# Kernel tuning notes

Hardware: AMD Instinct MI355X
Metric: run time of the kernel (lower is better)

## Reference

```python
import jax, jax.numpy as jnp
import numpy as np
from jax import lax

B = 8; DIM = 256; NH = 8; PATCH = 8; WS = 28; STRIDE = 8; PAD = 14; ORF = 2.0; IMG = 448


def conv2d(x, w, stride, pad, groups=1):
    return lax.conv_general_dilated(
        x, w, (stride, stride), [(pad, pad), (pad, pad)],
        dimension_numbers=('NCHW', 'OIHW', 'NCHW'), feature_group_count=groups)


def ln_ch(x, g, b):
    # LayerNormProxy: LayerNorm over channel dim of NCHW
    m = jnp.mean(x, 1, keepdims=True)
    v = jnp.mean((x - m) ** 2, 1, keepdims=True)
    return (x - m) * lax.rsqrt(v + 1e-5) * g[None, :, None, None] + b[None, :, None, None]


def bilinear_sample(x, grid):
    # x: (N,C,H,W); grid: (N,Hg,Wg,2) in (x,y) order, [-1,1], align_corners=True, zeros padding
    N, C, H, W = x.shape
    gx = (grid[..., 0] + 1.0) * 0.5 * (W - 1)
    gy = (grid[..., 1] + 1.0) * 0.5 * (H - 1)
    x0 = jnp.floor(gx); y0 = jnp.floor(gy)
    x1 = x0 + 1.0; y1 = y0 + 1.0
    wx1 = gx - x0; wx0 = 1.0 - wx1
    wy1 = gy - y0; wy0 = 1.0 - wy1
    xf = x.reshape(N, C, H * W)

    def corner(ix, iy, w):
        valid = (ix >= 0) & (ix <= W - 1) & (iy >= 0) & (iy <= H - 1)
        ii = (jnp.clip(iy, 0, H - 1) * W + jnp.clip(ix, 0, W - 1)).astype(jnp.int32).reshape(N, -1)
        vals = jax.vmap(lambda f, i: f[:, i])(xf, ii)  # (N,C,Hg*Wg)
        return vals * (w * valid).reshape(N, 1, -1)

    out = (corner(x0, y0, wx0 * wy0) + corner(x1, y0, wx1 * wy0)
           + corner(x0, y1, wx0 * wy1) + corner(x1, y1, wx1 * wy1))
    return out.reshape(N, C, grid.shape[1], grid.shape[2])


def setup_inputs() -> dict:
    key = jax.random.key(0)
    ks = jax.random.split(key, 12)
    s = 0.02
    CG = 64
    return {
        'x': jax.random.normal(ks[0], (B, 3, IMG, IMG), jnp.float32),
        'patch_w': jax.random.normal(ks[1], (DIM, 3, PATCH, PATCH), jnp.float32) * s,
        'patch_b': jnp.zeros((DIM,), jnp.float32),
        'ln1_g': jnp.ones((DIM,), jnp.float32),
        'ln1_b': jnp.zeros((DIM,), jnp.float32),
        'wq': jax.random.normal(ks[2], (DIM, DIM), jnp.float32) * s,
        'bq': jnp.zeros((DIM,), jnp.float32),
        'wk': jax.random.normal(ks[3], (DIM, DIM), jnp.float32) * s,
        'bk': jnp.zeros((DIM,), jnp.float32),
        'wv': jax.random.normal(ks[4], (DIM, DIM), jnp.float32) * s,
        'bv': jnp.zeros((DIM,), jnp.float32),
        'wo': jax.random.normal(ks[5], (DIM, DIM), jnp.float32) * s,
        'bo': jnp.zeros((DIM,), jnp.float32),
        'off_dw_w': jax.random.normal(ks[6], (CG, 1, WS, WS), jnp.float32) * s,
        'off_dw_b': jnp.zeros((CG,), jnp.float32),
        'off_ln_g': jnp.ones((CG,), jnp.float32),
        'off_ln_b': jnp.zeros((CG,), jnp.float32),
        'off_pw_w': jax.random.normal(ks[7], (2, CG), jnp.float32) * s,
        'rpe_w1': jax.random.normal(ks[8], (32, 2), jnp.float32) * 0.1,
        'rpe_b1': jnp.zeros((32,), jnp.float32),
        'rpe_w2': jax.random.normal(ks[9], (2, 32), jnp.float32) * 0.1,
    }


def reference(x, patch_w, patch_b, ln1_g, ln1_b, wq, bq, wk, bk, wv, bv, wo, bo,
              off_dw_w, off_dw_b, off_ln_g, off_ln_b, off_pw_w, rpe_w1, rpe_b1, rpe_w2):
    Bn = x.shape[0]
    # patch embedding: Conv2d(3, dim, patch, patch) + LayerNormProxy
    feat = conv2d(x, patch_w, PATCH, 0) + patch_b[None, :, None, None]
    feat = ln_ch(feat, ln1_g, ln1_b)
    H, W = feat.shape[2], feat.shape[3]  # 56, 56
    G = (H // WS) * (W // WS)            # 4 groups
    CG = DIM // G; GH = NH // G; HC = DIM // NH
    # q projection (1x1 conv)
    q = jnp.einsum('oc,bchw->bohw', wq, feat) + bq[None, :, None, None]
    # offset network on per-group query features
    q_off = q.reshape(Bn * G, CG, H, W)
    off = conv2d(q_off, off_dw_w, STRIDE, PAD, groups=CG) + off_dw_b[None, :, None, None]
    off = jax.nn.gelu(ln_ch(off, off_ln_g, off_ln_b), approximate=False)
    off = jnp.einsum('oc,bchw->bohw', off_pw_w, off)   # (B*G, 2, Hk, Wk)
    Hk, Wk = off.shape[2], off.shape[3]
    ns = Hk * Wk
    rng = jnp.array([1.0 / (Hk - 1), 1.0 / (Wk - 1)], off.dtype).reshape(1, 2, 1, 1)
    offset = jnp.tanh(off) * rng * ORF
    offset = jnp.transpose(offset, (0, 2, 3, 1))  # (B*G, Hk, Wk, 2) in (y, x)
    # reference points, normalized to ~[-1, 1]
    ry = jnp.linspace(0.5, Hk - 0.5, Hk) / (Hk - 1) * 2.0 - 1.0
    rx = jnp.linspace(0.5, Wk - 0.5, Wk) / (Wk - 1) * 2.0 - 1.0
    ref = jnp.stack(jnp.meshgrid(ry, rx, indexing='ij'), -1)  # (Hk, Wk, 2)
    ref = jnp.broadcast_to(ref[None], (Bn * G, Hk, Wk, 2))
    pos = offset + ref
    # deformable sampling (grid expects (x, y) order)
    xs = bilinear_sample(feat.reshape(Bn * G, CG, H, W), pos[..., ::-1])  # (B*G, CG, Hk, Wk)
    xs = xs.reshape(Bn, DIM, ns)
    k = jnp.einsum('oc,bcn->bon', wk, xs) + bk[None, :, None]
    v = jnp.einsum('oc,bcn->bon', wv, xs) + bv[None, :, None]
    qh = q.reshape(Bn * NH, HC, H * W)
    kh = k.reshape(Bn * NH, HC, ns)
    vh = v.reshape(Bn * NH, HC, ns)
    attn = jnp.einsum('bcm,bcn->bmn', qh, kh) * (HC ** -0.5)  # (B*NH, HW, ns)
    # log-CPB relative position bias
    qy = jnp.linspace(0.0, float(H), H) / (H - 1) * 2.0 - 1.0
    qx = jnp.linspace(0.0, float(W), W) / (W - 1) * 2.0 - 1.0
    qg = jnp.stack(jnp.meshgrid(qy, qx, indexing='ij'), -1).reshape(H * W, 2)
    disp = (qg[None, :, None, :] - pos.reshape(Bn * G, ns, 2)[:, None, :, :]) * 4.0
    disp = jnp.sign(disp) * jnp.log2(jnp.abs(disp) + 1.0) / 3.0  # /log2(8)
    bias = jax.nn.relu(jnp.einsum('bmnc,hc->bmnh', disp, rpe_w1) + rpe_b1)
    bias = jnp.einsum('bmnh,oh->bmno', bias, rpe_w2)  # (B*G, HW, ns, GH)
    attn = attn + jnp.transpose(bias, (0, 3, 1, 2)).reshape(Bn * NH, H * W, ns)
    attn = jax.nn.softmax(attn, axis=-1)
    out = jnp.einsum('bmn,bcn->bcm', attn, vh).reshape(Bn, DIM, H, W)
    y = jnp.einsum('oc,bchw->bohw', wo, out) + bo[None, :, None, None]
    return (y, pos.reshape(Bn, G, Hk, Wk, 2), ref.reshape(Bn, G, Hk, Wk, 2))
```

## Files before the change

### kernel.cpp

```cpp
#include <hip/hip_runtime.h>
#include <cstddef>


typedef short bf16x8 __attribute__((ext_vector_type(8)));
typedef float f32x4 __attribute__((ext_vector_type(4)));

static __device__ __forceinline__ ushort f2bf(float f) {
  union { float f; unsigned u; } v; v.f = f;
  unsigned r = v.u + 0x7fffu + ((v.u >> 16) & 1u);
  return (ushort)(r >> 16);
}
static __device__ __forceinline__ float bf2f(ushort u) {
  union { unsigned u; float f; } v; v.u = ((unsigned)u) << 16;
  return v.f;
}

#define OFF_FEATB 0u
#define OFF_QPK   3211264u
#define OFF_Q     6422528u
#define OFF_POS   12845056u
#define OFF_XS    12849152u
#define OFF_KPK   12980224u
#define OFF_VPK   13045760u
#define OFF_PWP   13111296u
#define OFF_WQP   13135872u
#define OFF_WOP   13168640u
#define OFF_WKT   13201408u
#define OFF_WVT   13266944u

__global__ __launch_bounds__(256) void k_xcvt(
    const float* __restrict__ x, ushort* __restrict__ xb) {
  const size_t i0 = ((size_t)blockIdx.x * 256 + threadIdx.x) * 8;
  float4 v0 = *(const float4*)(x + i0);
  float4 v1 = *(const float4*)(x + i0 + 4);
  bf16x8 o;
  o[0] = (short)f2bf(v0.x); o[1] = (short)f2bf(v0.y);
  o[2] = (short)f2bf(v0.z); o[3] = (short)f2bf(v0.w);
  o[4] = (short)f2bf(v1.x); o[5] = (short)f2bf(v1.y);
  o[6] = (short)f2bf(v1.z); o[7] = (short)f2bf(v1.w);
  *(bf16x8*)(xb + i0) = o;
}

__global__ __launch_bounds__(256) void k_pack(
    const float* __restrict__ pw, const float* __restrict__ wq,
    const float* __restrict__ wk, const float* __restrict__ wv,
    const float* __restrict__ wo, ushort* __restrict__ pwp,
    ushort* __restrict__ wqp, ushort* __restrict__ wop,
    float* __restrict__ wkT, float* __restrict__ wvT) {
  const int o = blockIdx.x, t = threadIdx.x, m = blockIdx.y;
  if (m == 0) {
    if (t < 192) pwp[((t >> 3) * 256 + o) * 8 + (t & 7)] = f2bf(pw[o * 192 + t]);
  } else if (m == 1) {
    wqp[((t >> 3) * 256 + o) * 8 + (t & 7)] = f2bf(wq[o * 256 + t]);
  } else if (m == 2) {
    wop[((t >> 3) * 256 + o) * 8 + (t & 7)] = f2bf(wo[o * 256 + t]);
  } else if (m == 3) {
    wkT[t * 256 + o] = wk[o * 256 + t];
  } else {
    wvT[t * 256 + o] = wv[o * 256 + t];
  }
}

__global__ __launch_bounds__(256) void k_patch_mfma(
    const ushort* __restrict__ xb, const ushort* __restrict__ pwp,
    const float* __restrict__ pb, const float* __restrict__ g1,
    const float* __restrict__ b1, ushort* __restrict__ featb) {
  const int t = threadIdx.x;
  const int lane = t & 63;
  const int wid = t >> 6;
  const int m_base = blockIdx.x * 64 + wid * 16;
  const int kg = lane >> 4;
  const int lr = lane & 15;
  const int mA = m_base + lr;
  const int bA = mA / 3136;
  const int posA = mA - bA * 3136;
  const int ohA = posA / 56;
  const int owA = posA - ohA * 56;

  f32x4 acc[16];
#pragma unroll
  for (int f = 0; f < 16; f++) {
    float bv = pb[f * 16 + lr];
    acc[f] = (f32x4){bv, bv, bv, bv};
  }
#pragma unroll
  for (int ks = 0; ks < 6; ks++) {
    const int k8 = ks * 4 + kg;
    const int ci = k8 >> 3, ii = k8 & 7;
    bf16x8 a = *(const bf16x8*)(xb +
        (((size_t)bA * 3 + ci) * 448 + (ohA * 8 + ii)) * 448 + owA * 8);
#pragma unroll
    for (int f = 0; f < 16; f++) {
      bf16x8 bfr = *(const bf16x8*)(pwp + (size_t)(k8 * 256 + f * 16 + lr) * 8);
      acc[f] = __builtin_amdgcn_mfma_f32_16x16x32_bf16(a, bfr, acc[f], 0, 0, 0);
    }
  }
  float mean[4], rstd[4];
#pragma unroll
  for (int j = 0; j < 4; j++) {
    float s1 = 0.f, s2 = 0.f;
#pragma unroll
    for (int f = 0; f < 16; f++) { float v = acc[f][j]; s1 += v; s2 += v * v; }
#pragma unroll
    for (int off = 8; off >= 1; off >>= 1) {
      s1 += __shfl_xor(s1, off);
      s2 += __shfl_xor(s2, off);
    }
    float mn = s1 * (1.f / 256.f);
    float var = s2 * (1.f / 256.f) - mn * mn;
    mean[j] = mn; rstd[j] = rsqrtf(var + 1e-5f);
  }
#pragma unroll
  for (int f = 0; f < 16; f++) {
    const int c = f * 16 + lr;
    const float gg = g1[c], bb = b1[c];
#pragma unroll
    for (int j = 0; j < 4; j++) {
      const int mo = m_base + kg * 4 + j;
      float v = (acc[f][j] - mean[j]) * rstd[j] * gg + bb;
      featb[(size_t)mo * 256 + c] = f2bf(v);
    }
  }
}

__global__ __launch_bounds__(512) void k_gemm_mfma(
    const ushort* __restrict__ apk, const ushort* __restrict__ wp,
    const float* __restrict__ bias, float* __restrict__ out,
    ushort* __restrict__ opk) {
  const int t = threadIdx.x;
  const int lane = t & 63;
  const int wid = t >> 6;
  const int mt = wid >> 1, nh = wid & 1;
  const int lr = lane & 15, kg = lane >> 4;
  const int m_base = blockIdx.x * 64 + mt * 16;
  const int mA = m_base + lr;

  f32x4 acc[8];
#pragma unroll
  for (int f = 0; f < 8; f++) {
    float bv = bias[nh * 128 + f * 16 + lr];
    acc[f] = (f32x4){bv, bv, bv, bv};
  }
  const ushort* arow = apk + (size_t)mA * 256;
#pragma unroll
  for (int ks = 0; ks < 8; ks++) {
    bf16x8 a = *(const bf16x8*)(arow + ks * 32 + kg * 8);
#pragma unroll
    for (int f = 0; f < 8; f++) {
      const int o = nh * 128 + f * 16 + lr;
      bf16x8 bfr = *(const bf16x8*)(wp + (size_t)((ks * 4 + kg) * 256 + o) * 8);
      acc[f] = __builtin_amdgcn_mfma_f32_16x16x32_bf16(a, bfr, acc[f], 0, 0, 0);
    }
  }
  __shared__ float sA[64 * 257];
#pragma unroll
  for (int f = 0; f < 8; f++) {
#pragma unroll
    for (int j = 0; j < 4; j++)
      sA[(mt * 16 + kg * 4 + j) * 257 + nh * 128 + f * 16 + lr] = acc[f][j];
  }
  __syncthreads();
  const int b = (blockIdx.x * 64) / 3136;
  const int pos0 = (blockIdx.x * 64) % 3136;
#pragma unroll
  for (int i = 0; i < 32; i++) {
    int idx = t + i * 512;
    int c = idx >> 6, mm = idx & 63;
    out[((size_t)b * 256 + c) * 3136 + pos0 + mm] = sA[mm * 257 + c];
  }
  if (opk) {
    const int mm = t & 63;
    const int cs = t >> 6;
#pragma unroll
    for (int i = 0; i < 4; i++) {
      int c0 = cs * 32 + i * 8;
      bf16x8 v8;
#pragma unroll
      for (int j = 0; j < 8; j++) v8[j] = (short)f2bf(sA[mm * 257 + c0 + j]);
      *(bf16x8*)(opk + ((size_t)(blockIdx.x * 64 + mm)) * 256 + c0) = v8;
    }
  }
}

__global__ __launch_bounds__(128) void k_offset_conv(
    const float* __restrict__ q, const float* __restrict__ dww,
    float* __restrict__ convo) {
  const int bg = blockIdx.y;
  const int wv = threadIdx.x >> 6;
  const int lane = threadIdx.x & 63;
  const int ch = blockIdx.x * 2 + wv;
  const int b = bg >> 2, g = bg & 3;

  __shared__ float pl[2][7072];
  float* P = pl[wv];
  for (int idx = lane; idx < 7072; idx += 64) P[idx] = 0.f;

  const float* qb = q + ((size_t)b * 256 + g * 64 + ch) * 3136;
  if (lane < 56) {
    for (int r = 0; r < 56; r++) {
      int hr = r + 14;
      P[hr * 84 + (lane + 14) + (hr >> 3)] = qb[r * 56 + lane];
    }
  }
  const int oh = lane >> 3, ow = lane & 7;
  const int chs = __builtin_amdgcn_readfirstlane(ch);
  const float* wr = dww + (size_t)chs * 784;
  float acc = 0.f;
  const int r0 = oh * 8, c0 = ow * 8;
  for (int i = 0; i < 28; i++) {
    int hr = r0 + i;
    const float* prow = P + hr * 84 + c0 + (hr >> 3);
    const float* wrr = wr + i * 28;
#pragma unroll
    for (int j = 0; j < 28; j++)
      acc = fmaf(prow[j], wrr[j], acc);
  }
  convo[bg * 4096 + lane * 64 + ch] = acc;
}

__global__ __launch_bounds__(256) void k_offset_post(
    const float* __restrict__ convo, const float* __restrict__ dwb,
    const float* __restrict__ lng, const float* __restrict__ lnb,
    const float* __restrict__ pww, float* __restrict__ pos_ws,
    float* __restrict__ out_pos, float* __restrict__ out_ref) {
  const int bg = blockIdx.y;
  const int wv = threadIdx.x >> 6;
  const int lane = threadIdx.x & 63;
  const int idx = blockIdx.x * 4 + wv;
  const int oh = idx >> 3, ow = idx & 7;

  float acc = convo[bg * 4096 + idx * 64 + lane] + dwb[lane];

  float s1 = acc, s2 = acc * acc;
#pragma unroll
  for (int off = 32; off >= 1; off >>= 1) {
    s1 += __shfl_xor(s1, off);
    s2 += __shfl_xor(s2, off);
  }
  float m = s1 * (1.f / 64.f);
  float var = s2 * (1.f / 64.f) - m * m;
  float val = (acc - m) * rsqrtf(var + 1e-5f) * lng[lane] + lnb[lane];
  val = 0.5f * val * (1.f + erff(val * 0.70710678118654752f));
  float p0 = pww[lane] * val, p1 = pww[64 + lane] * val;
#pragma unroll
  for (int off = 32; off >= 1; off >>= 1) {
    p0 += __shfl_xor(p0, off);
    p1 += __shfl_xor(p1, off);
  }
  if (lane == 0) {
    float offy = tanhf(p0) * (2.0f / 7.0f);
    float offx = tanhf(p1) * (2.0f / 7.0f);
    float ry = (0.5f + oh) * (2.0f / 7.0f) - 1.0f;
    float rx = (0.5f + ow) * (2.0f / 7.0f) - 1.0f;
    float py = offy + ry, px = offx + rx;
    int o = bg * 128 + idx * 2;
    pos_ws[o] = py;  pos_ws[o + 1] = px;
    out_pos[o] = py; out_pos[o + 1] = px;
    out_ref[o] = ry; out_ref[o + 1] = rx;
  }
}

__global__ __launch_bounds__(256) void k_sample_kv(
    const ushort* __restrict__ featb, const float* __restrict__ pos_ws,
    const float* __restrict__ wkT, const float* __restrict__ bk,
    const float* __restrict__ wvT, const float* __restrict__ bv,
    ushort* __restrict__ kpk, ushort* __restrict__ vpk) {
  const int b = blockIdx.y;
  const int n = blockIdx.x;
  const int t = threadIdx.x;
  const int g = t >> 6, lane = t & 63;
  const int bg = b * 4 + g;

  __shared__ float sxs[256];
  {
    float py = pos_ws[bg * 128 + n * 2];
    float px = pos_ws[bg * 128 + n * 2 + 1];
    float gx = (px + 1.f) * 0.5f * 55.f;
    float gy = (py + 1.f) * 0.5f * 55.f;
    float x0f = floorf(gx), y0f = floorf(gy);
    int x0 = (int)x0f, y0 = (int)y0f;
    float wx1 = gx - x0f, wx0 = 1.f - wx1;
    float wy1 = gy - y0f, wy0 = 1.f - wy1;
    const size_t mb = (size_t)b * 3136;
    const int cofs = g * 64 + lane;
    float acc = 0.f;
    if (x0 >= 0 && x0 <= 55 && y0 >= 0 && y0 <= 55)
      acc = fmaf(bf2f(featb[(mb + y0 * 56 + x0) * 256 + cofs]), wx0 * wy0, acc);
    if (x0 + 1 >= 0 && x0 + 1 <= 55 && y0 >= 0 && y0 <= 55)
      acc = fmaf(bf2f(featb[(mb + y0 * 56 + x0 + 1) * 256 + cofs]), wx1 * wy0, acc);
    if (x0 >= 0 && x0 <= 55 && y0 + 1 >= 0 && y0 + 1 <= 55)
      acc = fmaf(bf2f(featb[(mb + (y0 + 1) * 56 + x0) * 256 + cofs]), wx0 * wy1, acc);
    if (x0 + 1 >= 0 && x0 + 1 <= 55 && y0 + 1 >= 0 && y0 + 1 <= 55)
      acc = fmaf(bf2f(featb[(mb + (y0 + 1) * 56 + x0 + 1) * 256 + cofs]), wx1 * wy1, acc);
    sxs[g * 64 + lane] = acc;
  }
  __syncthreads();

  float ak = bk[t], av = bv[t];
  for (int c = 0; c < 256; c++) {
    float xv = sxs[c];
    ak = fmaf(wkT[c * 256 + t], xv, ak);
    av = fmaf(wvT[c * 256 + t], xv, av);
  }
  const int h = t >> 5, cc = t & 31;
  const size_t base = (size_t)(b * 8 + h) * 2048;
  kpk[base + (size_t)((cc >> 3) * 64 + n) * 8 + (cc & 7)] = f2bf(ak);
  vpk[base + (size_t)((n >> 3) * 32 + cc) * 8 + (n & 7)] = f2bf(av);
}

__global__ __launch_bounds__(256) void k_attn_mfma(
    const ushort* __restrict__ qpk, const ushort* __restrict__ kpk,
    const ushort* __restrict__ vpk, const float* __restrict__ pos_ws,
    const float* __restrict__ w1, const float* __restrict__ b1,
    const float* __restrict__ w2, ushort* __restrict__ attnpk) {
  const int bg = blockIdx.y;
  const int b = bg >> 2, g = bg & 3;
  const int m0 = blockIdx.x * 64;
  const int t = threadIdx.x;
  const int lane = t & 63, w = t >> 6;
  const int lr = lane & 15, kg = lane >> 4;

  __shared__ ushort Pbuf[4][16 * 72];
  __shared__ ushort outb[64 * 72];
  __shared__ float posl[128];
  __shared__ float4 rpe4[32];
  __shared__ float rpeB[32];

  if (t < 128) posl[t] = pos_ws[bg * 128 + t];
  if (t < 32) {
    rpe4[t] = make_float4(w1[t * 2], w1[t * 2 + 1], b1[t], w2[t]);
    rpeB[t] = w2[32 + t];
  }
  __syncthreads();

  float qgy[4], qgx[4];
#pragma unroll
  for (int j = 0; j < 4; j++) {
    int m = m0 + w * 16 + kg * 4 + j;
    int my = m / 56, mx = m % 56;
    qgy[j] = (float)my * (56.0f / 55.0f) * (2.0f / 55.0f) - 1.0f;
    qgx[j] = (float)mx * (56.0f / 55.0f) * (2.0f / 55.0f) - 1.0f;
  }
  float tyv[16], txv[16];
#pragma unroll
  for (int nf = 0; nf < 4; nf++) {
    int n = nf * 16 + lr;
    float py = posl[2 * n], px = posl[2 * n + 1];
#pragma unroll
    for (int j = 0; j < 4; j++) {
      float dy = (qgy[j] - py) * 4.f;
      float dx = (qgx[j] - px) * 4.f;
      tyv[nf * 4 + j] = copysignf(__log2f(fabsf(dy) + 1.f) * (1.f / 3.f), dy);
      txv[nf * 4 + j] = copysignf(__log2f(fabsf(dx) + 1.f) * (1.f / 3.f), dx);
    }
  }
  float bb0[16], bb1[16];
#pragma unroll
  for (int p = 0; p < 16; p++) { bb0[p] = 0.f; bb1[p] = 0.f; }
  for (int jj = 0; jj < 32; jj++) {
    float4 r = rpe4[jj];
    float wb = rpeB[jj];
#pragma unroll
    for (int p = 0; p < 16; p++) {
      float hv = fmaxf(fmaf(r.x, tyv[p], fmaf(r.y, txv[p], r.z)), 0.f);
      bb0[p] = fmaf(r.w, hv, bb0[p]);
      bb1[p] = fmaf(wb, hv, bb1[p]);
    }
  }

  const int mrow = m0 + w * 16 + lr;
  const float scale = 0.17677669529663687f;
  ushort* pb = Pbuf[w];

  f32x4 oacc[2][2];
#pragma unroll
  for (int gh = 0; gh < 2; gh++)
#pragma unroll
    for (int cf = 0; cf < 2; cf++) oacc[gh][cf] = (f32x4){0.f, 0.f, 0.f, 0.f};

#pragma unroll
  for (int gh = 0; gh < 2; gh++) {
    bf16x8 a = *(const bf16x8*)(qpk +
        ((size_t)(b * 3136 + mrow) * 256 + g * 64 + gh * 32 + kg * 8));
    const ushort* kbase = kpk + (size_t)(b * 8 + g * 2 + gh) * 2048;
    f32x4 s[4];
#pragma unroll
    for (int nf = 0; nf < 4; nf++) {
      bf16x8 bfr = *(const bf16x8*)(kbase + (size_t)(kg * 64 + nf * 16 + lr) * 8);
      s[nf] = __builtin_amdgcn_mfma_f32_16x16x32_bf16(
          a, bfr, (f32x4){0.f, 0.f, 0.f, 0.f}, 0, 0, 0);
    }
#pragma unroll
    for (int nf = 0; nf < 4; nf++)
#pragma unroll
      for (int j = 0; j < 4; j++)
        s[nf][j] = fmaf(s[nf][j], scale,
                        gh ? bb1[nf * 4 + j] : bb0[nf * 4 + j]);
#pragma unroll
    for (int j = 0; j < 4; j++) {
      float m1 = fmaxf(fmaxf(s[0][j], s[1][j]), fmaxf(s[2][j], s[3][j]));
#pragma unroll
      for (int o = 8; o >= 1; o >>= 1) m1 = fmaxf(m1, __shfl_xor(m1, o));
      float ss = 0.f;
#pragma unroll
      for (int nf = 0; nf < 4; nf++) {
        float e = __expf(s[nf][j] - m1);
        s[nf][j] = e;
        ss += e;
      }
#pragma unroll
      for (int o = 8; o >= 1; o >>= 1) ss += __shfl_xor(ss, o);
      float inv = 1.f / ss;
#pragma unroll
      for (int nf = 0; nf < 4; nf++) s[nf][j] *= inv;
    }
#pragma unroll
    for (int nf = 0; nf < 4; nf++)
#pragma unroll
      for (int j = 0; j < 4; j++)
        pb[(kg * 4 + j) * 72 + nf * 16 + lr] = f2bf(s[nf][j]);
    const ushort* vbase = vpk + (size_t)(b * 8 + g * 2 + gh) * 2048;
#pragma unroll
    for (int ks = 0; ks < 2; ks++) {
      bf16x8 pa = *(const bf16x8*)(pb + lr * 72 + ks * 32 + kg * 8);
#pragma unroll
      for (int cf = 0; cf < 2; cf++) {
        bf16x8 vb = *(const bf16x8*)(vbase +
            (size_t)((ks * 4 + kg) * 32 + cf * 16 + lr) * 8);
        oacc[gh][cf] = __builtin_amdgcn_mfma_f32_16x16x32_bf16(
            pa, vb, oacc[gh][cf], 0, 0, 0);
      }
    }
  }

#pragma unroll
  for (int gh = 0; gh < 2; gh++)
#pragma unroll
    for (int cf = 0; cf < 2; cf++)
#pragma unroll
      for (int j = 0; j < 4; j++)
        outb[(w * 16 + kg * 4 + j) * 72 + gh * 32 + cf * 16 + lr] =
            f2bf(oacc[gh][cf][j]);
  __syncthreads();
#pragma unroll
  for (int r2 = 0; r2 < 2; r2++) {
    int row = (t >> 3) + r2 * 32;
    int chunk = t & 7;
    bf16x8 v8 = *(const bf16x8*)(outb + row * 72 + chunk * 8);
    *(bf16x8*)(attnpk +
               ((size_t)(b * 3136 + m0 + row) * 256 + g * 64 + chunk * 8)) = v8;
  }
}

extern "C" void kernel_launch(void* const* d_in, const int* in_sizes, int n_in,
                              void* d_out, int out_size, void* d_ws,
                              size_t ws_size, hipStream_t stream) {
  const float* x       = (const float*)d_in[0];
  const float* patch_w = (const float*)d_in[1];
  const float* patch_b = (const float*)d_in[2];
  const float* ln1_g   = (const float*)d_in[3];
  const float* ln1_b   = (const float*)d_in[4];
  const float* wq      = (const float*)d_in[5];
  const float* bq      = (const float*)d_in[6];
  const float* wk      = (const float*)d_in[7];
  const float* bk      = (const float*)d_in[8];
  const float* wv      = (const float*)d_in[9];
  const float* bv      = (const float*)d_in[10];
  const float* wo      = (const float*)d_in[11];
  const float* bo      = (const float*)d_in[12];
  const float* off_dw_w = (const float*)d_in[13];
  const float* off_dw_b = (const float*)d_in[14];
  const float* off_ln_g = (const float*)d_in[15];
  const float* off_ln_b = (const float*)d_in[16];
  const float* off_pw_w = (const float*)d_in[17];
  const float* rpe_w1  = (const float*)d_in[18];
  const float* rpe_b1  = (const float*)d_in[19];
  const float* rpe_w2  = (const float*)d_in[20];

  float* ws = (float*)d_ws;
  ushort* featb = (ushort*)(ws + OFF_FEATB);
  ushort* attnpk = featb;
  ushort* qpk = (ushort*)(ws + OFF_QPK);
  float* q    = ws + OFF_Q;
  ushort* xb  = (ushort*)(ws + OFF_Q);
  float* posw = ws + OFF_POS;
  float* convo = ws + OFF_XS;
  ushort* kpk = (ushort*)(ws + OFF_KPK);
  ushort* vpk = (ushort*)(ws + OFF_VPK);
  ushort* pwp = (ushort*)(ws + OFF_PWP);
  ushort* wqp = (ushort*)(ws + OFF_WQP);
  ushort* wop = (ushort*)(ws + OFF_WOP);
  float* wkT  = ws + OFF_WKT;
  float* wvT  = ws + OFF_WVT;

  float* y = (float*)d_out;
  float* out_pos = y + 6422528;
  float* out_ref = out_pos + 4096;

  hipLaunchKernelGGL(k_xcvt, dim3(2352), dim3(256), 0, stream, x, xb);
  hipLaunchKernelGGL(k_pack, dim3(256, 5), dim3(256), 0, stream,
                     patch_w, wq, wk, wv, wo, pwp, wqp, wop, wkT, wvT);
  hipLaunchKernelGGL(k_patch_mfma, dim3(392), dim3(256), 0, stream,
                     xb, pwp, patch_b, ln1_g, ln1_b, featb);
  hipLaunchKernelGGL(k_gemm_mfma, dim3(392), dim3(512), 0, stream,
                     featb, wqp, bq, q, qpk);
  hipLaunchKernelGGL(k_offset_conv, dim3(32, 32), dim3(128), 0, stream,
                     q, off_dw_w, convo);
  hipLaunchKernelGGL(k_offset_post, dim3(16, 32), dim3(256), 0, stream,
                     convo, off_dw_b, off_ln_g, off_ln_b, off_pw_w,
                     posw, out_pos, out_ref);
  hipLaunchKernelGGL(k_sample_kv, dim3(64, 8), dim3(256), 0, stream,
                     featb, posw, wkT, bk, wvT, bv, kpk, vpk);
  hipLaunchKernelGGL(k_attn_mfma, dim3(49, 32), dim3(256), 0, stream,
                     qpk, kpk, vpk, posw, rpe_w1, rpe_b1, rpe_w2, attnpk);
  hipLaunchKernelGGL(k_gemm_mfma, dim3(392), dim3(512), 0, stream,
                     attnpk, wop, bo, y, (ushort*)nullptr);
}
```

Measured before the change: 244.0 us.

## Stage weights in LDS, use MFMA for K/V projection, half-precision RPE MLP

The patch-embed and linear GEMM kernels now cover 128 rows per block and keep double-buffered weight tiles in shared memory, so B fragments are reused across two M sub-tiles instead of being reloaded from global memory. K/V sampling is restructured into one block per batch that does vectorized bilinear gathers into LDS and then a bf16 MFMA GEMM, replacing the per-sample scalar fp32 dot products. The relative-position-bias MLP in attention is moved to packed half2 arithmetic. The risks are fewer blocks (196 and 8) leaving the GPU underoccupied, especially the 8-block sample_kv, and lost precision in the fp16 bias.

```diff
diff --git a/kernel.cpp b/kernel.cpp
--- a/kernel.cpp
+++ b/kernel.cpp
@@ -1,4 +1,5 @@
 #include <hip/hip_runtime.h>
+#include <hip/hip_fp16.h>
 #include <cstddef>
 
 
@@ -13,6 +14,10 @@
 static __device__ __forceinline__ float bf2f(ushort u) {
   union { unsigned u; float f; } v; v.u = ((unsigned)u) << 16;
   return v.f;
+}
+static __device__ __forceinline__ __half2 h2max(__half2 a, __half2 b) {
+  return __halves2half2(__hmax(__low2half(a), __low2half(b)),
+                        __hmax(__high2half(a), __high2half(b)));
 }
 
 #define OFF_FEATB 0u
@@ -25,8 +30,8 @@
 #define OFF_PWP   13111296u
 #define OFF_WQP   13135872u
 #define OFF_WOP   13168640u
-#define OFF_WKT   13201408u
-#define OFF_WVT   13266944u
+#define OFF_WKP   13201408u
+#define OFF_WVP   13234176u
 
 __global__ __launch_bounds__(256) void k_xcvt(
     const float* __restrict__ x, ushort* __restrict__ xb) {
@@ -45,19 +50,15 @@
     const float* __restrict__ pw, const float* __restrict__ wq,
     const float* __restrict__ wk, const float* __restrict__ wv,
     const float* __restrict__ wo, ushort* __restrict__ pwp,
-    ushort* __restrict__ wqp, ushort* __restrict__ wop,
-    float* __restrict__ wkT, float* __restrict__ wvT) {
+    ushort* __restrict__ wqp, ushort* __restrict__ wkp,
+    ushort* __restrict__ wvp, ushort* __restrict__ wop) {
   const int o = blockIdx.x, t = threadIdx.x, m = blockIdx.y;
   if (m == 0) {
     if (t < 192) pwp[((t >> 3) * 256 + o) * 8 + (t & 7)] = f2bf(pw[o * 192 + t]);
-  } else if (m == 1) {
-    wqp[((t >> 3) * 256 + o) * 8 + (t & 7)] = f2bf(wq[o * 256 + t]);
-  } else if (m == 2) {
-    wop[((t >> 3) * 256 + o) * 8 + (t & 7)] = f2bf(wo[o * 256 + t]);
-  } else if (m == 3) {
-    wkT[t * 256 + o] = wk[o * 256 + t];
   } else {
-    wvT[t * 256 + o] = wv[o * 256 + t];
+    const float* in = (m == 1) ? wq : (m == 2) ? wk : (m == 3) ? wv : wo;
+    ushort* out = (m == 1) ? wqp : (m == 2) ? wkp : (m == 3) ? wvp : wop;
+    out[((t >> 3) * 256 + o) * 8 + (t & 7)] = f2bf(in[o * 256 + t]);
   }
 }
 
@@ -65,120 +66,195 @@
     const ushort* __restrict__ xb, const ushort* __restrict__ pwp,
     const float* __restrict__ pb, const float* __restrict__ g1,
     const float* __restrict__ b1, ushort* __restrict__ featb) {
+  __shared__ ushort Bs[2][8192];
   const int t = threadIdx.x;
-  const int lane = t & 63;
-  const int wid = t >> 6;
-  const int m_base = blockIdx.x * 64 + wid * 16;
-  const int kg = lane >> 4;
-  const int lr = lane & 15;
-  const int mA = m_base + lr;
-  const int bA = mA / 3136;
-  const int posA = mA - bA * 3136;
-  const int ohA = posA / 56;
-  const int owA = posA - ohA * 56;
-
-  f32x4 acc[16];
+  const int lane = t & 63, w = t >> 6;
+  const int lr = lane & 15, kg = lane >> 4;
+  const int m_base = blockIdx.x * 128 + w * 32;
+
+  size_t abase[2];
+#pragma unroll
+  for (int mr = 0; mr < 2; mr++) {
+    int mA = m_base + mr * 16 + lr;
+    int bA = mA / 3136;
+    int posA = mA - bA * 3136;
+    int ohA = posA / 56;
+    int owA = posA - ohA * 56;
+    abase[mr] = (((size_t)bA * 3) * 448 + ohA * 8) * 448 + owA * 8;
+  }
+
+  f32x4 acc[2][16];
 #pragma unroll
   for (int f = 0; f < 16; f++) {
     float bv = pb[f * 16 + lr];
-    acc[f] = (f32x4){bv, bv, bv, bv};
-  }
-#pragma unroll
+    acc[0][f] = (f32x4){bv, bv, bv, bv};
+    acc[1][f] = (f32x4){bv, bv, bv, bv};
+  }
+
+  bf16x8 st[4];
+#pragma unroll
+  for (int i = 0; i < 4; i++)
+    st[i] = *(const bf16x8*)(pwp + i * 2048 + t * 8);
+#pragma unroll
+  for (int i = 0; i < 4; i++)
+    *(bf16x8*)(&Bs[0][i * 2048 + t * 8]) = st[i];
+  __syncthreads();
+  int p = 0;
   for (int ks = 0; ks < 6; ks++) {
+    if (ks < 5) {
+#pragma unroll
+      for (int i = 0; i < 4; i++)
+        st[i] = *(const bf16x8*)(pwp + (ks + 1) * 8192 + i * 2048 + t * 8);
+    }
     const int k8 = ks * 4 + kg;
     const int ci = k8 >> 3, ii = k8 & 7;
-    bf16x8 a = *(const bf16x8*)(xb +
-        (((size_t)bA * 3 + ci) * 448 + (ohA * 8 + ii)) * 448 + owA * 8);
+    bf16x8 a0 = *(const bf16x8*)(xb + abase[0] + (size_t)ci * 200704 + ii * 448);
+    bf16x8 a1 = *(const bf16x8*)(xb + abase[1] + (size_t)ci * 200704 + ii * 448);
+    const ushort* bsl = &Bs[p][kg * 2048];
 #pragma unroll
     for (int f = 0; f < 16; f++) {
-      bf16x8 bfr = *(const bf16x8*)(pwp + (size_t)(k8 * 256 + f * 16 + lr) * 8);
-      acc[f] = __builtin_amdgcn_mfma_f32_16x16x32_bf16(a, bfr, acc[f], 0, 0, 0);
-    }
-  }
-  float mean[4], rstd[4];
-#pragma unroll
-  for (int j = 0; j < 4; j++) {
-    float s1 = 0.f, s2 = 0.f;
-#pragma unroll
-    for (int f = 0; f < 16; f++) { float v = acc[f][j]; s1 += v; s2 += v * v; }
-#pragma unroll
-    for (int off = 8; off >= 1; off >>= 1) {
-      s1 += __shfl_xor(s1, off);
-      s2 += __shfl_xor(s2, off);
-    }
-    float mn = s1 * (1.f / 256.f);
-    float var = s2 * (1.f / 256.f) - mn * mn;
-    mean[j] = mn; rstd[j] = rsqrtf(var + 1e-5f);
-  }
-#pragma unroll
-  for (int f = 0; f < 16; f++) {
-    const int c = f * 16 + lr;
-    const float gg = g1[c], bb = b1[c];
+      bf16x8 bfr = *(const bf16x8*)(bsl + (f * 16 + lr) * 8);
+      acc[0][f] = __builtin_amdgcn_mfma_f32_16x16x32_bf16(a0, bfr, acc[0][f], 0, 0, 0);
+      acc[1][f] = __builtin_amdgcn_mfma_f32_16x16x32_bf16(a1, bfr, acc[1][f], 0, 0, 0);
+    }
+    __syncthreads();
+    if (ks < 5) {
+#pragma unroll
+      for (int i = 0; i < 4; i++)
+        *(bf16x8*)(&Bs[p ^ 1][i * 2048 + t * 8]) = st[i];
+      __syncthreads();
+      p ^= 1;
+    }
+  }
+
+#pragma unroll
+  for (int mr = 0; mr < 2; mr++) {
+    float mean[4], rstd[4];
 #pragma unroll
     for (int j = 0; j < 4; j++) {
-      const int mo = m_base + kg * 4 + j;
-      float v = (acc[f][j] - mean[j]) * rstd[j] * gg + bb;
-      featb[(size_t)mo * 256 + c] = f2bf(v);
-    }
-  }
-}
-
-__global__ __launch_bounds__(512) void k_gemm_mfma(
+      float s1 = 0.f, s2 = 0.f;
+#pragma unroll
+      for (int f = 0; f < 16; f++) { float v = acc[mr][f][j]; s1 += v; s2 += v * v; }
+#pragma unroll
+      for (int off = 8; off >= 1; off >>= 1) {
+        s1 += __shfl_xor(s1, off);
+        s2 += __shfl_xor(s2, off);
+      }
+      float mn = s1 * (1.f / 256.f);
+      float var = s2 * (1.f / 256.f) - mn * mn;
+      mean[j] = mn; rstd[j] = rsqrtf(var + 1e-5f);
+    }
+#pragma unroll
+    for (int f = 0; f < 16; f++) {
+      const int c = f * 16 + lr;
+      const float gg = g1[c], bb = b1[c];
+#pragma unroll
+      for (int j = 0; j < 4; j++) {
+        const int mo = m_base + mr * 16 + kg * 4 + j;
+        float v = (acc[mr][f][j] - mean[j]) * rstd[j] * gg + bb;
+        featb[(size_t)mo * 256 + c] = f2bf(v);
+      }
+    }
+  }
+}
+
+__global__ __launch_bounds__(256) void k_gemm_mfma(
     const ushort* __restrict__ apk, const ushort* __restrict__ wp,
     const float* __restrict__ bias, float* __restrict__ out,
     ushort* __restrict__ opk) {
+  __shared__ float smem[16448];
+  ushort* Bs = (ushort*)smem;
+  float* sA = smem;
   const int t = threadIdx.x;
-  const int lane = t & 63;
-  const int wid = t >> 6;
-  const int mt = wid >> 1, nh = wid & 1;
+  const int lane = t & 63, w = t >> 6;
   const int lr = lane & 15, kg = lane >> 4;
-  const int m_base = blockIdx.x * 64 + mt * 16;
-  const int mA = m_base + lr;
-
-  f32x4 acc[8];
-#pragma unroll
-  for (int f = 0; f < 8; f++) {
-    float bv = bias[nh * 128 + f * 16 + lr];
-    acc[f] = (f32x4){bv, bv, bv, bv};
-  }
-  const ushort* arow = apk + (size_t)mA * 256;
-#pragma unroll
+  const int m_base = blockIdx.x * 128 + w * 32;
+
+  f32x4 acc[2][16];
+#pragma unroll
+  for (int f = 0; f < 16; f++) {
+    float bv = bias[f * 16 + lr];
+    acc[0][f] = (f32x4){bv, bv, bv, bv};
+    acc[1][f] = (f32x4){bv, bv, bv, bv};
+  }
+  const ushort* a0p = apk + (size_t)(m_base + lr) * 256;
+  const ushort* a1p = a0p + 16 * 256;
+
+  bf16x8 st[4];
+#pragma unroll
+  for (int i = 0; i < 4; i++) st[i] = *(const bf16x8*)(wp + i * 2048 + t * 8);
+#pragma unroll
+  for (int i = 0; i < 4; i++) *(bf16x8*)(Bs + i * 2048 + t * 8) = st[i];
+  __syncthreads();
+  int p = 0;
   for (int ks = 0; ks < 8; ks++) {
-    bf16x8 a = *(const bf16x8*)(arow + ks * 32 + kg * 8);
-#pragma unroll
-    for (int f = 0; f < 8; f++) {
-      const int o = nh * 128 + f * 16 + lr;
-      bf16x8 bfr = *(const bf16x8*)(wp + (size_t)((ks * 4 + kg) * 256 + o) * 8);
-      acc[f] = __builtin_amdgcn_mfma_f32_16x16x32_bf16(a, bfr, acc[f], 0, 0, 0);
-    }
-  }
-  __shared__ float sA[64 * 257];
-#pragma unroll
-  for (int f = 0; f < 8; f++) {
-#pragma unroll
-    for (int j = 0; j < 4; j++)
-      sA[(mt * 16 + kg * 4 + j) * 257 + nh * 128 + f * 16 + lr] = acc[f][j];
+    if (ks < 7) {
+#pragma unroll
+      for (int i = 0; i < 4; i++)
+        st[i] = *(const bf16x8*)(wp + (ks + 1) * 8192 + i * 2048 + t * 8);
+    }
+    bf16x8 a0 = *(const bf16x8*)(a0p + ks * 32 + kg * 8);
+    bf16x8 a1 = *(const bf16x8*)(a1p + ks * 32 + kg * 8);
+    const ushort* bsl = Bs + p * 8192 + kg * 2048;
+#pragma unroll
+    for (int f = 0; f < 16; f++) {
+      bf16x8 bfr = *(const bf16x8*)(bsl + (f * 16 + lr) * 8);
+      acc[0][f] = __builtin_amdgcn_mfma_f32_16x16x32_bf16(a0, bfr, acc[0][f], 0, 0, 0);
+      acc[1][f] = __builtin_amdgcn_mfma_f32_16x16x32_bf16(a1, bfr, acc[1][f], 0, 0, 0);
+    }
+    __syncthreads();
+    if (ks < 7) {
+#pragma unroll
+      for (int i = 0; i < 4; i++)
+        *(bf16x8*)(Bs + (p ^ 1) * 8192 + i * 2048 + t * 8) = st[i];
+      __syncthreads();
+      p ^= 1;
+    }
   }
   __syncthreads();
-  const int b = (blockIdx.x * 64) / 3136;
-  const int pos0 = (blockIdx.x * 64) % 3136;
-#pragma unroll
-  for (int i = 0; i < 32; i++) {
-    int idx = t + i * 512;
-    int c = idx >> 6, mm = idx & 63;
-    out[((size_t)b * 256 + c) * 3136 + pos0 + mm] = sA[mm * 257 + c];
-  }
-  if (opk) {
-    const int mm = t & 63;
-    const int cs = t >> 6;
-#pragma unroll
-    for (int i = 0; i < 4; i++) {
-      int c0 = cs * 32 + i * 8;
-      bf16x8 v8;
-#pragma unroll
-      for (int j = 0; j < 8; j++) v8[j] = (short)f2bf(sA[mm * 257 + c0 + j]);
-      *(bf16x8*)(opk + ((size_t)(blockIdx.x * 64 + mm)) * 256 + c0) = v8;
-    }
+
+#pragma unroll
+  for (int h = 0; h < 2; h++) {
+    if ((w >> 1) == h) {
+      const int loc0 = (w & 1) * 32;
+#pragma unroll
+      for (int mr = 0; mr < 2; mr++)
+#pragma unroll
+        for (int f = 0; f < 16; f++)
+#pragma unroll
+          for (int j = 0; j < 4; j++)
+            sA[(loc0 + mr * 16 + kg * 4 + j) * 257 + f * 16 + lr] = acc[mr][f][j];
+    }
+    __syncthreads();
+    const int R0 = blockIdx.x * 128 + h * 64;
+    const int bh = R0 / 3136;
+    const int pos0 = R0 % 3136;
+    {
+      const int c = t;
+      float* op = out + ((size_t)bh * 256 + c) * 3136 + pos0;
+#pragma unroll
+      for (int i4 = 0; i4 < 16; i4++) {
+        float4 v;
+        v.x = sA[(i4 * 4 + 0) * 257 + c];
+        v.y = sA[(i4 * 4 + 1) * 257 + c];
+        v.z = sA[(i4 * 4 + 2) * 257 + c];
+        v.w = sA[(i4 * 4 + 3) * 257 + c];
+        *(float4*)(op + i4 * 4) = v;
+      }
+    }
+    if (opk) {
+      const int mm = t & 63, cs = t >> 6;
+      const int c0 = cs * 64;
+#pragma unroll
+      for (int jj = 0; jj < 8; jj++) {
+        bf16x8 v8;
+#pragma unroll
+        for (int e = 0; e < 8; e++)
+          v8[e] = (short)f2bf(sA[mm * 257 + c0 + jj * 8 + e]);
+        *(bf16x8*)(opk + (size_t)(R0 + mm) * 256 + c0 + jj * 8) = v8;
+      }
+    }
+    __syncthreads();
   }
 }
 
@@ -260,52 +336,105 @@
   }
 }
 
-__global__ __launch_bounds__(256) void k_sample_kv(
+__global__ __launch_bounds__(512) void k_sample_kv(
     const ushort* __restrict__ featb, const float* __restrict__ pos_ws,
-    const float* __restrict__ wkT, const float* __restrict__ bk,
-    const float* __restrict__ wvT, const float* __restrict__ bv,
+    const ushort* __restrict__ wkp, const float* __restrict__ bk,
+    const ushort* __restrict__ wvp, const float* __restrict__ bv,
     ushort* __restrict__ kpk, ushort* __restrict__ vpk) {
-  const int b = blockIdx.y;
-  const int n = blockIdx.x;
+  const int b = blockIdx.x;
   const int t = threadIdx.x;
-  const int g = t >> 6, lane = t & 63;
-  const int bg = b * 4 + g;
-
-  __shared__ float sxs[256];
+  __shared__ ushort xsb[64 * 264];
+  __shared__ ushort Cst[2][64 * 264];
+
   {
+    const int n = t >> 3, c0 = (t & 7) * 32;
+    const int g = c0 >> 6;
+    const int bg = b * 4 + g;
     float py = pos_ws[bg * 128 + n * 2];
     float px = pos_ws[bg * 128 + n * 2 + 1];
-    float gx = (px + 1.f) * 0.5f * 55.f;
-    float gy = (py + 1.f) * 0.5f * 55.f;
+    float gx = (px + 1.f) * 27.5f;
+    float gy = (py + 1.f) * 27.5f;
     float x0f = floorf(gx), y0f = floorf(gy);
     int x0 = (int)x0f, y0 = (int)y0f;
     float wx1 = gx - x0f, wx0 = 1.f - wx1;
     float wy1 = gy - y0f, wy0 = 1.f - wy1;
-    const size_t mb = (size_t)b * 3136;
-    const int cofs = g * 64 + lane;
-    float acc = 0.f;
-    if (x0 >= 0 && x0 <= 55 && y0 >= 0 && y0 <= 55)
-      acc = fmaf(bf2f(featb[(mb + y0 * 56 + x0) * 256 + cofs]), wx0 * wy0, acc);
-    if (x0 + 1 >= 0 && x0 + 1 <= 55 && y0 >= 0 && y0 <= 55)
-      acc = fmaf(bf2f(featb[(mb + y0 * 56 + x0 + 1) * 256 + cofs]), wx1 * wy0, acc);
-    if (x0 >= 0 && x0 <= 55 && y0 + 1 >= 0 && y0 + 1 <= 55)
-      acc = fmaf(bf2f(featb[(mb + (y0 + 1) * 56 + x0) * 256 + cofs]), wx0 * wy1, acc);
-    if (x0 + 1 >= 0 && x0 + 1 <= 55 && y0 + 1 >= 0 && y0 + 1 <= 55)
-      acc = fmaf(bf2f(featb[(mb + (y0 + 1) * 56 + x0 + 1) * 256 + cofs]), wx1 * wy1, acc);
-    sxs[g * 64 + lane] = acc;
+    float v00 = (x0 >= 0 && x0 <= 55 && y0 >= 0 && y0 <= 55) ? 1.f : 0.f;
+    float v01 = (x0 + 1 >= 0 && x0 + 1 <= 55 && y0 >= 0 && y0 <= 55) ? 1.f : 0.f;
+    float v10 = (x0 >= 0 && x0 <= 55 && y0 + 1 >= 0 && y0 + 1 <= 55) ? 1.f : 0.f;
+    float v11 = (x0 + 1 >= 0 && x0 + 1 <= 55 && y0 + 1 >= 0 && y0 + 1 <= 55) ? 1.f : 0.f;
+    float w00 = wx0 * wy0 * v00, w01 = wx1 * wy0 * v01;
+    float w10 = wx0 * wy1 * v10, w11 = wx1 * wy1 * v11;
+    int cx0 = min(max(x0, 0), 55), cx1 = min(max(x0 + 1, 0), 55);
+    int cy0 = min(max(y0, 0), 55), cy1 = min(max(y0 + 1, 0), 55);
+    const ushort* fb = featb + (size_t)b * 3136 * 256;
+    const ushort* p00 = fb + (size_t)(cy0 * 56 + cx0) * 256;
+    const ushort* p01 = fb + (size_t)(cy0 * 56 + cx1) * 256;
+    const ushort* p10 = fb + (size_t)(cy1 * 56 + cx0) * 256;
+    const ushort* p11 = fb + (size_t)(cy1 * 56 + cx1) * 256;
+#pragma unroll
+    for (int q4 = 0; q4 < 4; q4++) {
+      const int c = c0 + q4 * 8;
+      bf16x8 a00 = *(const bf16x8*)(p00 + c);
+      bf16x8 a01 = *(const bf16x8*)(p01 + c);
+      bf16x8 a10 = *(const bf16x8*)(p10 + c);
+      bf16x8 a11 = *(const bf16x8*)(p11 + c);
+      bf16x8 o8;
+#pragma unroll
+      for (int e = 0; e < 8; e++) {
+        float s = bf2f((ushort)a00[e]) * w00 + bf2f((ushort)a01[e]) * w01 +
+                  bf2f((ushort)a10[e]) * w10 + bf2f((ushort)a11[e]) * w11;
+        o8[e] = (short)f2bf(s);
+      }
+      *(bf16x8*)(xsb + n * 264 + c) = o8;
+    }
   }
   __syncthreads();
 
-  float ak = bk[t], av = bv[t];
-  for (int c = 0; c < 256; c++) {
-    float xv = sxs[c];
-    ak = fmaf(wkT[c * 256 + t], xv, ak);
-    av = fmaf(wvT[c * 256 + t], xv, av);
-  }
-  const int h = t >> 5, cc = t & 31;
-  const size_t base = (size_t)(b * 8 + h) * 2048;
-  kpk[base + (size_t)((cc >> 3) * 64 + n) * 8 + (cc & 7)] = f2bf(ak);
-  vpk[base + (size_t)((n >> 3) * 32 + cc) * 8 + (n & 7)] = f2bf(av);
+  const int lane = t & 63, w = t >> 6;
+  const int mat = w >> 2, mt = w & 3;
+  const int lr = lane & 15, kg = lane >> 4;
+  const ushort* wp = mat ? wvp : wkp;
+  const float* bs = mat ? bv : bk;
+  f32x4 acc[16];
+#pragma unroll
+  for (int f = 0; f < 16; f++) {
+    float bvv = bs[f * 16 + lr];
+    acc[f] = (f32x4){bvv, bvv, bvv, bvv};
+  }
+#pragma unroll
+  for (int ks = 0; ks < 8; ks++) {
+    bf16x8 a = *(const bf16x8*)(xsb + (mt * 16 + lr) * 264 + ks * 32 + kg * 8);
+#pragma unroll
+    for (int f = 0; f < 16; f++) {
+      bf16x8 bfr = *(const bf16x8*)(wp + (size_t)((ks * 4 + kg) * 256 + f * 16 + lr) * 8);
+      acc[f] = __builtin_amdgcn_mfma_f32_16x16x32_bf16(a, bfr, acc[f], 0, 0, 0);
+    }
+  }
+  ushort* cst = Cst[mat];
+#pragma unroll
+  for (int f = 0; f < 16; f++)
+#pragma unroll
+    for (int j = 0; j < 4; j++)
+      cst[(mt * 16 + kg * 4 + j) * 264 + f * 16 + lr] = f2bf(acc[f][j]);
+  __syncthreads();
+
+#pragma unroll
+  for (int pass = 0; pass < 4; pass++) {
+    int grp = pass * 8 + (t >> 6);
+    int h = grp >> 2, c8 = grp & 3, n2 = t & 63;
+    bf16x8 v8 = *(const bf16x8*)(Cst[0] + n2 * 264 + h * 32 + c8 * 8);
+    *(bf16x8*)(kpk + (size_t)(b * 8 + h) * 2048 + (c8 * 64 + n2) * 8) = v8;
+  }
+#pragma unroll
+  for (int pass = 0; pass < 4; pass++) {
+    int grp = pass * 512 + t;
+    int h = grp >> 8, n8 = (grp >> 5) & 7, cc = grp & 31;
+    bf16x8 v8;
+#pragma unroll
+    for (int e = 0; e < 8; e++)
+      v8[e] = (short)Cst[1][(n8 * 8 + e) * 264 + h * 32 + cc];
+    *(bf16x8*)(vpk + (size_t)(b * 8 + h) * 2048 + (n8 * 32 + cc) * 8) = v8;
+  }
 }
 
 __global__ __launch_bounds__(256) void k_attn_mfma(
@@ -323,13 +452,15 @@
   __shared__ ushort Pbuf[4][16 * 72];
   __shared__ ushort outb[64 * 72];
   __shared__ float posl[128];
-  __shared__ float4 rpe4[32];
-  __shared__ float rpeB[32];
+  __shared__ __half2 rpeh[32][6];
 
   if (t < 128) posl[t] = pos_ws[bg * 128 + t];
   if (t < 32) {
-    rpe4[t] = make_float4(w1[t * 2], w1[t * 2 + 1], b1[t], w2[t]);
-    rpeB[t] = w2[32 + t];
+    rpeh[t][0] = __float2half2_rn(w1[t * 2]);
+    rpeh[t][1] = __float2half2_rn(w1[t * 2 + 1]);
+    rpeh[t][2] = __float2half2_rn(b1[t]);
+    rpeh[t][3] = __float2half2_rn(w2[t]);
+    rpeh[t][4] = __float2half2_rn(w2[32 + t]);
   }
   __syncthreads();
 
@@ -354,18 +485,32 @@
       txv[nf * 4 + j] = copysignf(__log2f(fabsf(dx) + 1.f) * (1.f / 3.f), dx);
     }
   }
+  __half2 ty2[8], tx2[8], bb02[8], bb12[8];
+  const __half2 z2 = __float2half2_rn(0.f);
+#pragma unroll
+  for (int k = 0; k < 8; k++) {
+    ty2[k] = __floats2half2_rn(tyv[2 * k], tyv[2 * k + 1]);
+    tx2[k] = __floats2half2_rn(txv[2 * k], txv[2 * k + 1]);
+    bb02[k] = z2; bb12[k] = z2;
+  }
+  for (int jj = 0; jj < 32; jj++) {
+    __half2 hy = rpeh[jj][0], hx = rpeh[jj][1], hb = rpeh[jj][2];
+    __half2 ha = rpeh[jj][3], hc = rpeh[jj][4];
+#pragma unroll
+    for (int k = 0; k < 8; k++) {
+      __half2 h = __hfma2(hy, ty2[k], __hfma2(hx, tx2[k], hb));
+      h = h2max(h, z2);
+      bb02[k] = __hfma2(ha, h, bb02[k]);
+      bb12[k] = __hfma2(hc, h, bb12[k]);
+    }
+  }
   float bb0[16], bb1[16];
 #pragma unroll
-  for (int p = 0; p < 16; p++) { bb0[p] = 0.f; bb1[p] = 0.f; }
-  for (int jj = 0; jj < 32; jj++) {
-    float4 r = rpe4[jj];
-    float wb = rpeB[jj];
-#pragma unroll
-    for (int p = 0; p < 16; p++) {
-      float hv = fmaxf(fmaf(r.x, tyv[p], fmaf(r.y, txv[p], r.z)), 0.f);
-      bb0[p] = fmaf(r.w, hv, bb0[p]);
-      bb1[p] = fmaf(wb, hv, bb1[p]);
-    }
+  for (int k = 0; k < 8; k++) {
+    float2 f0 = __half22float2(bb02[k]);
+    float2 f1 = __half22float2(bb12[k]);
+    bb0[2 * k] = f0.x; bb0[2 * k + 1] = f0.y;
+    bb1[2 * k] = f1.x; bb1[2 * k + 1] = f1.y;
   }
 
   const int mrow = m0 + w * 16 + lr;
@@ -490,8 +635,8 @@
   ushort* pwp = (ushort*)(ws + OFF_PWP);
   ushort* wqp = (ushort*)(ws + OFF_WQP);
   ushort* wop = (ushort*)(ws + OFF_WOP);
-  float* wkT  = ws + OFF_WKT;
-  float* wvT  = ws + OFF_WVT;
+  ushort* wkp = (ushort*)(ws + OFF_WKP);
+  ushort* wvp = (ushort*)(ws + OFF_WVP);
 
   float* y = (float*)d_out;
   float* out_pos = y + 6422528;
@@ -499,20 +644,20 @@
 
   hipLaunchKernelGGL(k_xcvt, dim3(2352), dim3(256), 0, stream, x, xb);
   hipLaunchKernelGGL(k_pack, dim3(256, 5), dim3(256), 0, stream,
-                     patch_w, wq, wk, wv, wo, pwp, wqp, wop, wkT, wvT);
-  hipLaunchKernelGGL(k_patch_mfma, dim3(392), dim3(256), 0, stream,
+                     patch_w, wq, wk, wv, wo, pwp, wqp, wkp, wvp, wop);
+  hipLaunchKernelGGL(k_patch_mfma, dim3(196), dim3(256), 0, stream,
                      xb, pwp, patch_b, ln1_g, ln1_b, featb);
-  hipLaunchKernelGGL(k_gemm_mfma, dim3(392), dim3(512), 0, stream,
+  hipLaunchKernelGGL(k_gemm_mfma, dim3(196), dim3(256), 0, stream,
                      featb, wqp, bq, q, qpk);
   hipLaunchKernelGGL(k_offset_conv, dim3(32, 32), dim3(128), 0, stream,
                      q, off_dw_w, convo);
   hipLaunchKernelGGL(k_offset_post, dim3(16, 32), dim3(256), 0, stream,
                      convo, off_dw_b, off_ln_g, off_ln_b, off_pw_w,
                      posw, out_pos, out_ref);
-  hipLaunchKernelGGL(k_sample_kv, dim3(64, 8), dim3(256), 0, stream,
-                     featb, posw, wkT, bk, wvT, bv, kpk, vpk);
+  hipLaunchKernelGGL(k_sample_kv, dim3(8), dim3(512), 0, stream,
+                     featb, posw, wkp, bk, wvp, bv, kpk, vpk);
   hipLaunchKernelGGL(k_attn_mfma, dim3(49, 32), dim3(256), 0, stream,
                      qpk, kpk, vpk, posw, rpe_w1, rpe_b1, rpe_w2, attnpk);
-  hipLaunchKernelGGL(k_gemm_mfma, dim3(392), dim3(512), 0, stream,
+  hipLaunchKernelGGL(k_gemm_mfma, dim3(196), dim3(256), 0, stream,
                      attnpk, wop, bo, y, (ushort*)nullptr);
 }
```

Result: slower. 279.5 us (+14.6%).
